# Kernel optimization log

Hardware: AMD Instinct MI355X
Metric: run time of the kernel (lower is better)

Reference implementation:

```python
import math
import jax, jax.numpy as jnp
import numpy as np

B, T, C, H = 2, 2048, 1024, 16
HD = C // H  # head dim = 64
EPS_LN = 1e-5
EPS_ENT = 1e-8


def layer_norm(x, w, b):
    mu = jnp.mean(x, axis=-1, keepdims=True)
    var = jnp.var(x, axis=-1, keepdims=True)
    return (x - mu) * jax.lax.rsqrt(var + EPS_LN) * w + b


def new_gelu(x):
    c = math.sqrt(2.0 / math.pi)
    return 0.5 * x * (1.0 + jnp.tanh(c * (x + 0.044715 * x * x * x)))


def setup_inputs() -> dict:
    key = jax.random.key(0)
    ks = jax.random.split(key, 8)
    s = 0.02
    return {
        "x": jax.random.normal(ks[0], (B, T, C), dtype=jnp.float32),
        "ln1_w": jnp.ones((C,), jnp.float32),
        "ln1_b": jnp.zeros((C,), jnp.float32),
        "w_attn": jax.random.normal(ks[1], (3 * C, C), jnp.float32) * s,
        "b_attn": jnp.zeros((3 * C,), jnp.float32),
        "w_proj": jax.random.normal(ks[2], (C, C), jnp.float32) * s,
        "b_proj": jnp.zeros((C,), jnp.float32),
        "ln2_w": jnp.ones((C,), jnp.float32),
        "ln2_b": jnp.zeros((C,), jnp.float32),
        "w_fc": jax.random.normal(ks[3], (4 * C, C), jnp.float32) * s,
        "b_fc": jnp.zeros((4 * C,), jnp.float32),
        "w_mlp": jax.random.normal(ks[4], (C, 4 * C), jnp.float32) * s,
        "b_mlp": jnp.zeros((C,), jnp.float32),
    }


def reference(x, ln1_w, ln1_b, w_attn, b_attn, w_proj, b_proj,
              ln2_w, ln2_b, w_fc, b_fc, w_mlp, b_mlp):
    # --- attention branch (pre-LN) ---
    h = layer_norm(x, ln1_w, ln1_b)
    qkv = h @ w_attn.T + b_attn                      # (B,T,3C)
    q, k, v = jnp.split(qkv, 3, axis=-1)
    # (B,T,C) -> (B,H,T,HD)
    q = q.reshape(B, T, H, HD).transpose(0, 2, 1, 3)
    k = k.reshape(B, T, H, HD).transpose(0, 2, 1, 3)
    v = v.reshape(B, T, H, HD).transpose(0, 2, 1, 3)

    att = jnp.einsum('bhqd,bhkd->bhqk', q, k) * (1.0 / math.sqrt(HD))
    causal = jnp.tril(jnp.ones((T, T), dtype=bool))
    att = jnp.where(causal, att, -jnp.inf)
    att = jax.nn.softmax(att, axis=-1)               # (B,H,T,T)
    # entropy per query, averaged over batch/heads/positions -> scalar
    att_entropy = jnp.mean(jnp.sum(-att * jnp.log(att + EPS_ENT), axis=-1))

    y = jnp.einsum('bhqk,bhkd->bhqd', att, v)        # (B,H,T,HD)
    y = y.transpose(0, 2, 1, 3).reshape(B, T, C)
    y = y @ w_proj.T + b_proj
    x = x + y

    # --- MLP branch ---
    h2 = layer_norm(x, ln2_w, ln2_b)
    m = new_gelu(h2 @ w_fc.T + b_fc) @ w_mlp.T + b_mlp
    x = x + m

    present = jnp.stack([k, v])                      # (2,B,H,T,HD)
    return (x, att_entropy, present)
```

## Files before the change

### kernel.cpp

```cpp
#include <hip/hip_runtime.h>
#include <hip/hip_bf16.h>
#include <stdint.h>


typedef __bf16 bf16x8 __attribute__((ext_vector_type(8)));
typedef __bf16 bf16x4 __attribute__((ext_vector_type(4)));
typedef float  f32x4  __attribute__((ext_vector_type(4)));

#define GLDS16(g, l)                                                          \
  __builtin_amdgcn_global_load_lds(                                           \
      (__attribute__((address_space(1))) void*)(g),                           \
      (__attribute__((address_space(3))) void*)(l), 16, 0, 0)

__device__ __forceinline__ float gelu_f(float x) {
  float u2 = 1.5957691216057308f * (x + 0.044715f * x * x * x);
  return x * __builtin_amdgcn_rcpf(1.0f + __expf(-u2));
}

__global__ __launch_bounds__(256) void cast_w(
    const float* s0, const float* s1, const float* s2, const float* s3,
    __bf16* d0, __bf16* d1, __bf16* d2, __bf16* d3,
    int n0, int n1, int n2, int n3) {
  int a = blockIdx.y;
  const float* s = (a == 0) ? s0 : (a == 1) ? s1 : (a == 2) ? s2 : s3;
  __bf16* d      = (a == 0) ? d0 : (a == 1) ? d1 : (a == 2) ? d2 : d3;
  int n          = (a == 0) ? n0 : (a == 1) ? n1 : (a == 2) ? n2 : n3;
  int i = (blockIdx.x * 256 + threadIdx.x) * 4;
  if (i < n) {
    float4 v = *(const float4*)(s + i);
    bf16x4 o = {(__bf16)v.x, (__bf16)v.y, (__bf16)v.z, (__bf16)v.w};
    *(bf16x4*)(d + i) = o;
  }
}

__global__ __launch_bounds__(256) void ln_kernel(
    const float* __restrict__ x, const float* __restrict__ gw,
    const float* __restrict__ gb, __bf16* __restrict__ out) {
  const int row = blockIdx.x, tid = threadIdx.x;
  const float4 v = ((const float4*)(x + (size_t)row * 1024))[tid];
  float s = v.x + v.y + v.z + v.w;
  float sq = v.x * v.x + v.y * v.y + v.z * v.z + v.w * v.w;
#pragma unroll
  for (int m = 1; m < 64; m <<= 1) {
    s += __shfl_xor(s, m, 64);
    sq += __shfl_xor(sq, m, 64);
  }
  __shared__ float red[8];
  if ((tid & 63) == 0) { red[tid >> 6] = s; red[4 + (tid >> 6)] = sq; }
  __syncthreads();
  s = red[0] + red[1] + red[2] + red[3];
  sq = red[4] + red[5] + red[6] + red[7];
  const float mu = s * (1.0f / 1024.0f);
  const float var = sq * (1.0f / 1024.0f) - mu * mu;
  const float rs = rsqrtf(var + 1e-5f);
  const float4 wv = ((const float4*)gw)[tid];
  const float4 bv = ((const float4*)gb)[tid];
  bf16x4 o;
  o[0] = (__bf16)((v.x - mu) * rs * wv.x + bv.x);
  o[1] = (__bf16)((v.y - mu) * rs * wv.y + bv.y);
  o[2] = (__bf16)((v.z - mu) * rs * wv.z + bv.z);
  o[3] = (__bf16)((v.w - mu) * rs * wv.w + bv.w);
  *(bf16x4*)(out + (size_t)row * 1024 + tid * 4) = o;
}

template <int EPI, int BN, int MINW>
__global__ __launch_bounds__(256, MINW) void gemm_bt(
    const __bf16* __restrict__ A, const __bf16* __restrict__ Bw,
    const float* __restrict__ bias, const float* __restrict__ resid,
    float* __restrict__ outF, __bf16* __restrict__ outH, int M, int N, int K) {
  __shared__ __bf16 As[2][128 * 32];
  __shared__ __bf16 Bs[2][BN * 32];
  constexpr int JN = BN / 32;
  const int tid = threadIdx.x;
  const int w = tid >> 6, lane = tid & 63, l15 = lane & 15, quad = lane >> 4;
  const int wm = (w >> 1) * 64, wn = (w & 1) * (BN / 2);
  const int nx = gridDim.x;
  const int j = blockIdx.y * nx + blockIdx.x;
  const int xcd = j & 7, u = j >> 3;
  const int yl = u / nx, xx = u - yl * nx;
  const int yy = xcd * (gridDim.y >> 3) + yl;
  const int m0 = yy * 128, n0 = xx * BN;
  const int arow = tid >> 2, acol = (tid & 3) * 8;

  f32x4 acc[4][JN] = {};

  const __bf16* ga = A + (size_t)(m0 + arow) * K + acol;
  const __bf16* gb = Bw + (size_t)(n0 + arow) * K + acol;
  for (int k0 = 0; k0 < K; k0 += 64) {
    __syncthreads();
#pragma unroll
    for (int h = 0; h < 2; ++h) {
      GLDS16(ga + k0 + h * 32, (char*)As[h] + tid * 16);
      GLDS16(ga + k0 + h * 32 + (size_t)64 * K, (char*)As[h] + 4096 + tid * 16);
      GLDS16(gb + k0 + h * 32, (char*)Bs[h] + tid * 16);
      if (BN == 128)
        GLDS16(gb + k0 + h * 32 + (size_t)64 * K,
               (char*)Bs[h] + 4096 + tid * 16);
    }
    __syncthreads();
#pragma unroll
    for (int h = 0; h < 2; ++h) {
      bf16x8 af[4], bfr[JN];
#pragma unroll
      for (int i = 0; i < 4; ++i)
        af[i] = *(const bf16x8*)(As[h] + (wm + i * 16 + l15) * 32 + quad * 8);
#pragma unroll
      for (int j2 = 0; j2 < JN; ++j2)
        bfr[j2] = *(const bf16x8*)(Bs[h] + (wn + j2 * 16 + l15) * 32 + quad * 8);
#pragma unroll
      for (int i = 0; i < 4; ++i)
#pragma unroll
        for (int j2 = 0; j2 < JN; ++j2)
          acc[i][j2] = __builtin_amdgcn_mfma_f32_16x16x32_bf16(
              bfr[j2], af[i], acc[i][j2], 0, 0, 0);
    }
  }
#pragma unroll
  for (int j2 = 0; j2 < JN; ++j2) {
    const int nb = n0 + wn + j2 * 16 + quad * 4;
    const float4 bv = *(const float4*)(bias + nb);
#pragma unroll
    for (int i = 0; i < 4; ++i) {
      const int m = m0 + wm + i * 16 + l15;
      const size_t idx = (size_t)m * N + nb;
      const float v0 = acc[i][j2][0] + bv.x;
      const float v1 = acc[i][j2][1] + bv.y;
      const float v2 = acc[i][j2][2] + bv.z;
      const float v3 = acc[i][j2][3] + bv.w;
      if (EPI == 0) {
        bf16x4 o = {(__bf16)v0, (__bf16)v1, (__bf16)v2, (__bf16)v3};
        *(bf16x4*)(outH + idx) = o;
      } else if (EPI == 1) {
        const float4 rv = *(const float4*)(resid + idx);
        float4 o = {v0 + rv.x, v1 + rv.y, v2 + rv.z, v3 + rv.w};
        *(float4*)(outF + idx) = o;
      } else {
        bf16x4 o = {(__bf16)gelu_f(v0), (__bf16)gelu_f(v1), (__bf16)gelu_f(v2),
                    (__bf16)gelu_f(v3)};
        *(bf16x4*)(outH + idx) = o;
      }
    }
  }
}

__global__ __launch_bounds__(256) void prep_kernel(
    const __bf16* __restrict__ qkv, __bf16* __restrict__ Qb,
    __bf16* __restrict__ Kb, __bf16* __restrict__ Vtb,
    float* __restrict__ pres) {
  const int tt = blockIdx.x, bh = blockIdx.y;
  const int b = bh >> 4, h = bh & 15;
  const int t0 = tt * 64, tid = threadIdx.x;
  const int r = tid >> 2, c = (tid & 3) * 16;
  __shared__ __bf16 Vs[64 * 72];

  const __bf16* base = qkv + (size_t)(b * 2048 + t0 + r) * 3072 + h * 64 + c;
  bf16x8 q0 = *(const bf16x8*)(base);
  bf16x8 q1 = *(const bf16x8*)(base + 8);
  bf16x8 k0 = *(const bf16x8*)(base + 1024);
  bf16x8 k1 = *(const bf16x8*)(base + 1032);
  bf16x8 v0 = *(const bf16x8*)(base + 2048);
  bf16x8 v1 = *(const bf16x8*)(base + 2056);

  const size_t orow = ((size_t)bh * 2048 + t0 + r) * 64 + c;
  *(bf16x8*)(Qb + orow) = q0;
  *(bf16x8*)(Qb + orow + 8) = q1;
  *(bf16x8*)(Kb + orow) = k0;
  *(bf16x8*)(Kb + orow + 8) = k1;

  float* pk = pres + (((size_t)(b * 16 + h)) * 2048 + t0 + r) * 64 + c;
  float* pv = pk + (size_t)2 * 16 * 2048 * 64;
#pragma unroll
  for (int i = 0; i < 4; ++i) {
    float4 fk = {(float)k0[i * 4 + 0], (float)k0[i * 4 + 1],
                 (float)k0[i * 4 + 2], (float)k0[i * 4 + 3]};
    float4 fv = {(float)v0[i * 4 + 0], (float)v0[i * 4 + 1],
                 (float)v0[i * 4 + 2], (float)v0[i * 4 + 3]};
    if (i >= 2) {
      fk = {(float)k1[i * 4 - 8], (float)k1[i * 4 - 7], (float)k1[i * 4 - 6],
            (float)k1[i * 4 - 5]};
      fv = {(float)v1[i * 4 - 8], (float)v1[i * 4 - 7], (float)v1[i * 4 - 6],
            (float)v1[i * 4 - 5]};
    }
    ((float4*)pk)[i] = fk;
    ((float4*)pv)[i] = fv;
  }

  *(bf16x8*)(Vs + r * 72 + c) = v0;
  *(bf16x8*)(Vs + r * 72 + c + 8) = v1;
  __syncthreads();
  const int d = tid >> 2, tc = (tid & 3) * 16;
  bf16x8 o0, o1;
#pragma unroll
  for (int i = 0; i < 8; ++i) {
    o0[i] = Vs[(tc + i) * 72 + d];
    o1[i] = Vs[(tc + 8 + i) * 72 + d];
  }
  __bf16* vo = Vtb + ((size_t)bh * 64 + d) * 2048 + t0 + tc;
  *(bf16x8*)(vo) = o0;
  *(bf16x8*)(vo + 8) = o1;
}

__global__ __launch_bounds__(256) void attn_kernel(
    const __bf16* __restrict__ Qb, const __bf16* __restrict__ Kb,
    const __bf16* __restrict__ Vtb, __bf16* __restrict__ attn_out,
    float* __restrict__ ent_acc) {
  const int jlin = blockIdx.y * 16 + blockIdx.x;
  const int xcd = jlin & 7, u = jlin >> 3;
  const int qp = u & 15;
  const int bh = xcd * 4 + (u >> 4);
  const int b = bh >> 4, h = bh & 15;
  const int tid = threadIdx.x, w = tid >> 6, lane = tid & 63;
  const int l15 = lane & 15, quad = lane >> 4;

  __shared__ __bf16 Ks[64 * 72];
  __shared__ __bf16 Vt[64 * 72];
  __shared__ __bf16 Ps[64 * 72];
  __shared__ float entred[4];

  const __bf16* qbase = Qb + (size_t)bh * 2048 * 64;
  const __bf16* kbase = Kb + (size_t)bh * 2048 * 64;
  const __bf16* vbase = Vtb + (size_t)bh * 64 * 2048;

  const int sr = tid >> 2, sc = (tid & 3) * 16;

  float hacc = 0.f;

#pragma unroll 1
  for (int ph = 0; ph < 2; ++ph) {
    const int qt = ph ? (31 - qp) : qp;
    const int q0 = qt * 64;
    const int qrow = q0 + w * 16 + l15;
    bf16x8 qf[2];
#pragma unroll
    for (int s = 0; s < 2; ++s)
      qf[s] = *(const bf16x8*)(qbase + (size_t)qrow * 64 + s * 32 + quad * 8);

    f32x4 O[4] = {};
    float m_s = -1e30f, l_s = 0.f, r_s = 0.f;

    for (int kt = 0; kt <= qt; ++kt) {
      const int kk0 = kt * 64;
      __syncthreads();
      {
        bf16x8 k0 = *(const bf16x8*)(kbase + (size_t)(kk0 + sr) * 64 + sc);
        bf16x8 k1 = *(const bf16x8*)(kbase + (size_t)(kk0 + sr) * 64 + sc + 8);
        bf16x8 v0 = *(const bf16x8*)(vbase + (size_t)sr * 2048 + kk0 + sc);
        bf16x8 v1 = *(const bf16x8*)(vbase + (size_t)sr * 2048 + kk0 + sc + 8);
        *(bf16x8*)(Ks + sr * 72 + sc) = k0;
        *(bf16x8*)(Ks + sr * 72 + sc + 8) = k1;
        *(bf16x8*)(Vt + sr * 72 + sc) = v0;
        *(bf16x8*)(Vt + sr * 72 + sc + 8) = v1;
      }
      __syncthreads();

      f32x4 sacc[4] = {};
#pragma unroll
      for (int s = 0; s < 2; ++s)
#pragma unroll
        for (int jt = 0; jt < 4; ++jt) {
          bf16x8 kf =
              *(const bf16x8*)(Ks + (jt * 16 + l15) * 72 + s * 32 + quad * 8);
          sacc[jt] =
              __builtin_amdgcn_mfma_f32_16x16x32_bf16(kf, qf[s], sacc[jt], 0, 0, 0);
        }

      float sv[4][4], ev[4][4];
#pragma unroll
      for (int jt = 0; jt < 4; ++jt)
#pragma unroll
        for (int r = 0; r < 4; ++r) {
          float xv = sacc[jt][r] * 0.125f;
          if (kk0 + jt * 16 + quad * 4 + r > qrow) xv = -1e30f;
          sv[jt][r] = xv;
        }
      float mx = sv[0][0];
#pragma unroll
      for (int jt = 0; jt < 4; ++jt)
#pragma unroll
        for (int r = 0; r < 4; ++r) mx = fmaxf(mx, sv[jt][r]);
      mx = fmaxf(mx, __shfl_xor(mx, 16, 64));
      mx = fmaxf(mx, __shfl_xor(mx, 32, 64));
      const float mn = fmaxf(m_s, mx);
      const float al = __expf(m_s - mn);
      m_s = mn;
      float ls = 0.f, rs2 = 0.f;
#pragma unroll
      for (int jt = 0; jt < 4; ++jt)
#pragma unroll
        for (int r = 0; r < 4; ++r) {
          const float e = __expf(sv[jt][r] - mn);
          ev[jt][r] = e;
          ls += e;
          rs2 = fmaf(e, sv[jt][r], rs2);
        }
      ls += __shfl_xor(ls, 16, 64);
      rs2 += __shfl_xor(rs2, 16, 64);
      ls += __shfl_xor(ls, 32, 64);
      rs2 += __shfl_xor(rs2, 32, 64);
      l_s = l_s * al + ls;
      r_s = r_s * al + rs2;
#pragma unroll
      for (int jt = 0; jt < 4; ++jt)
#pragma unroll
        for (int r = 0; r < 4; ++r) O[jt][r] *= al;

      __bf16* prow = Ps + (w * 16 + l15) * 72;
#pragma unroll
      for (int jt = 0; jt < 4; ++jt) {
        bf16x4 pk = {(__bf16)ev[jt][0], (__bf16)ev[jt][1], (__bf16)ev[jt][2],
                     (__bf16)ev[jt][3]};
        *(bf16x4*)(prow + jt * 16 + quad * 4) = pk;
      }
      asm volatile("s_waitcnt lgkmcnt(0)" ::: "memory");
#pragma unroll
      for (int s = 0; s < 2; ++s) {
        bf16x8 pf = *(const bf16x8*)(prow + s * 32 + quad * 8);
#pragma unroll
        for (int jt = 0; jt < 4; ++jt) {
          bf16x8 vf =
              *(const bf16x8*)(Vt + (jt * 16 + l15) * 72 + s * 32 + quad * 8);
          O[jt] = __builtin_amdgcn_mfma_f32_16x16x32_bf16(vf, pf, O[jt], 0, 0, 0);
        }
      }
    }

    const float inv = 1.0f / l_s;
    __bf16* obase = attn_out + (size_t)(b * 2048 + qrow) * 1024 + h * 64;
#pragma unroll
    for (int jt = 0; jt < 4; ++jt) {
      bf16x4 ov = {(__bf16)(O[jt][0] * inv), (__bf16)(O[jt][1] * inv),
                   (__bf16)(O[jt][2] * inv), (__bf16)(O[jt][3] * inv)};
      *(bf16x4*)(obase + jt * 16 + quad * 4) = ov;
    }
    hacc += m_s + __logf(l_s) - r_s * inv;
  }

#pragma unroll
  for (int m = 1; m < 64; m <<= 1) hacc += __shfl_xor(hacc, m, 64);
  if (lane == 0) entred[w] = hacc;
  __syncthreads();
  if (tid == 0)
    atomicAdd(ent_acc, (entred[0] + entred[1] + entred[2] + entred[3]) *
                           (1.0f / (4.0f * 65536.0f)));
}

__global__ void ent_final(const float* __restrict__ e, float* __restrict__ o) {
  if (threadIdx.x == 0) o[0] = e[0];
}

extern "C" void kernel_launch(void* const* d_in, const int* in_sizes, int n_in,
                              void* d_out, int out_size, void* d_ws,
                              size_t ws_size, hipStream_t stream) {
  const float* x      = (const float*)d_in[0];
  const float* ln1_w  = (const float*)d_in[1];
  const float* ln1_b  = (const float*)d_in[2];
  const float* w_attn = (const float*)d_in[3];
  const float* b_attn = (const float*)d_in[4];
  const float* w_proj = (const float*)d_in[5];
  const float* b_proj = (const float*)d_in[6];
  const float* ln2_w  = (const float*)d_in[7];
  const float* ln2_b  = (const float*)d_in[8];
  const float* w_fc   = (const float*)d_in[9];
  const float* b_fc   = (const float*)d_in[10];
  const float* w_mlp  = (const float*)d_in[11];
  const float* b_mlp  = (const float*)d_in[12];

  char* ws = (char*)d_ws;
  constexpr size_t MB = 1024ull * 1024ull;
  __bf16* qkv    = (__bf16*)(ws + 0);
  __bf16* act    = (__bf16*)(ws + 0);
  __bf16* wbattn = (__bf16*)(ws + 24 * MB);
  __bf16* wbproj = (__bf16*)(ws + 30 * MB);
  __bf16* attnb  = (__bf16*)(ws + 32 * MB);
  __bf16* hb     = (__bf16*)(ws + 40 * MB);
  __bf16* Vtb    = (__bf16*)(ws + 40 * MB);
  __bf16* Qb     = (__bf16*)(ws + 48 * MB);
  __bf16* Kb     = (__bf16*)(ws + 56 * MB);
  float*  x2     = (float*)(ws + 48 * MB);
  __bf16* wbfc   = (__bf16*)(ws + 64 * MB);
  __bf16* wbmlp  = (__bf16*)(ws + 72 * MB);
  float*  entw   = (float*)(ws + 80 * MB);

  float* xout   = (float*)d_out;
  float* entout = xout + 4194304;
  float* pres   = xout + 4194305;

  hipMemsetAsync(entw, 0, sizeof(float), stream);
  cast_w<<<dim3(4096, 4), 256, 0, stream>>>(
      w_attn, w_proj, w_fc, w_mlp, wbattn, wbproj, wbfc, wbmlp,
      3 * 1024 * 1024, 1024 * 1024, 4 * 1024 * 1024, 4 * 1024 * 1024);
  ln_kernel<<<4096, 256, 0, stream>>>(x, ln1_w, ln1_b, hb);
  gemm_bt<0, 128, 4><<<dim3(24, 32), 256, 0, stream>>>(
      hb, wbattn, b_attn, nullptr, nullptr, qkv, 4096, 3072, 1024);
  prep_kernel<<<dim3(32, 32), 256, 0, stream>>>(qkv, Qb, Kb, Vtb, pres);
  attn_kernel<<<dim3(16, 32), 256, 0, stream>>>(Qb, Kb, Vtb, attnb, entw);
  gemm_bt<1, 64, 2><<<dim3(16, 32), 256, 0, stream>>>(
      attnb, wbproj, b_proj, x, x2, nullptr, 4096, 1024, 1024);
  ln_kernel<<<4096, 256, 0, stream>>>(x2, ln2_w, ln2_b, hb);
  gemm_bt<2, 128, 4><<<dim3(32, 32), 256, 0, stream>>>(
      hb, wbfc, b_fc, nullptr, nullptr, act, 4096, 4096, 1024);
  gemm_bt<1, 64, 2><<<dim3(16, 32), 256, 0, stream>>>(
      act, wbmlp, b_mlp, x2, xout, nullptr, 4096, 1024, 4096);
  ent_final<<<1, 64, 0, stream>>>(entw, entout);
}
```

Baseline: 383.2 us.

## Double-buffer GEMM K-loop so the next tile loads during MFMA compute

Restructures the GEMM main loop from a load-all-then-compute pattern over two 32-wide halves into a software-pipelined double buffer. The next 32-wide K slab is prefetched into the alternate LDS buffer before computing on the current one, using explicit s_waitcnt vmcnt and s_barrier. This aims to hide global-to-LDS latency behind MFMA work. In exchange it runs twice as many loop iterations, each with two barriers, and relies on hand-counted vmcnt values that must match the number of outstanding loads.

```diff
diff --git a/kernel.cpp b/kernel.cpp
--- a/kernel.cpp
+++ b/kernel.cpp
@@ -86,34 +86,46 @@
 
   const __bf16* ga = A + (size_t)(m0 + arow) * K + acol;
   const __bf16* gb = Bw + (size_t)(n0 + arow) * K + acol;
-  for (int k0 = 0; k0 < K; k0 += 64) {
-    __syncthreads();
-#pragma unroll
-    for (int h = 0; h < 2; ++h) {
-      GLDS16(ga + k0 + h * 32, (char*)As[h] + tid * 16);
-      GLDS16(ga + k0 + h * 32 + (size_t)64 * K, (char*)As[h] + 4096 + tid * 16);
-      GLDS16(gb + k0 + h * 32, (char*)Bs[h] + tid * 16);
+
+  auto stage = [&](int k0, int buf) {
+    GLDS16(ga + k0, (char*)As[buf] + tid * 16);
+    GLDS16(ga + k0 + (size_t)64 * K, (char*)As[buf] + 4096 + tid * 16);
+    GLDS16(gb + k0, (char*)Bs[buf] + tid * 16);
+    if (BN == 128)
+      GLDS16(gb + k0 + (size_t)64 * K, (char*)Bs[buf] + 4096 + tid * 16);
+  };
+
+  stage(0, 0);
+  const int T = K >> 5;
+#pragma unroll 1
+  for (int t = 0; t < T; ++t) {
+    asm volatile("s_barrier" ::: "memory");
+    if (t + 1 < T) {
+      stage((t + 1) << 5, (t + 1) & 1);
       if (BN == 128)
-        GLDS16(gb + k0 + h * 32 + (size_t)64 * K,
-               (char*)Bs[h] + 4096 + tid * 16);
+        asm volatile("s_waitcnt vmcnt(4)" ::: "memory");
+      else
+        asm volatile("s_waitcnt vmcnt(3)" ::: "memory");
+    } else {
+      asm volatile("s_waitcnt vmcnt(0)" ::: "memory");
     }
-    __syncthreads();
-#pragma unroll
-    for (int h = 0; h < 2; ++h) {
-      bf16x8 af[4], bfr[JN];
-#pragma unroll
-      for (int i = 0; i < 4; ++i)
-        af[i] = *(const bf16x8*)(As[h] + (wm + i * 16 + l15) * 32 + quad * 8);
+    asm volatile("s_barrier" ::: "memory");
+
+    const __bf16* as = As[t & 1];
+    const __bf16* bs = Bs[t & 1];
+    bf16x8 af[4], bfr[JN];
+#pragma unroll
+    for (int i = 0; i < 4; ++i)
+      af[i] = *(const bf16x8*)(as + (wm + i * 16 + l15) * 32 + quad * 8);
+#pragma unroll
+    for (int j2 = 0; j2 < JN; ++j2)
+      bfr[j2] = *(const bf16x8*)(bs + (wn + j2 * 16 + l15) * 32 + quad * 8);
+#pragma unroll
+    for (int i = 0; i < 4; ++i)
 #pragma unroll
       for (int j2 = 0; j2 < JN; ++j2)
-        bfr[j2] = *(const bf16x8*)(Bs[h] + (wn + j2 * 16 + l15) * 32 + quad * 8);
-#pragma unroll
-      for (int i = 0; i < 4; ++i)
-#pragma unroll
-        for (int j2 = 0; j2 < JN; ++j2)
-          acc[i][j2] = __builtin_amdgcn_mfma_f32_16x16x32_bf16(
-              bfr[j2], af[i], acc[i][j2], 0, 0, 0);
-    }
+        acc[i][j2] = __builtin_amdgcn_mfma_f32_16x16x32_bf16(
+            bfr[j2], af[i], acc[i][j2], 0, 0, 0);
   }
 #pragma unroll
   for (int j2 = 0; j2 < JN; ++j2) {
```

Measured after the change: 395.7 us. 1.03x slower.
